# Kernel tuning notes

Hardware: AMD Instinct MI355X
Metric: run time of the kernel (lower is better)

The kernel has to match this reference:

```python
import jax, jax.numpy as jnp
import numpy as np

B, LX, LY, D = 8, 2048, 2048, 256

def setup_inputs() -> dict:
    key = jax.random.key(0)
    k1, k2, k3, k4 = jax.random.split(key, 4)
    x = jax.random.normal(k1, (B, LX, D), dtype=jnp.float32)
    y = jax.random.normal(k2, (B, LY, D), dtype=jnp.float32)
    y_mask = jax.random.randint(k3, (B, LY), 0, 2).astype(jnp.bool_)
    W = jax.random.normal(k4, (D, D), dtype=jnp.float32) * (1.0 / np.sqrt(D))
    b = jnp.zeros((D,), dtype=jnp.float32)
    return {"x": x, "y": y, "y_mask": y_mask, "W": W, "b": b}

def reference(x, y, y_mask, W, b):
    # shared linear + relu projection (torch Linear: x @ W.T + b)
    x_proj = jax.nn.relu(jnp.einsum('bld,ed->ble', x, W) + b)  # [B,LX,D]
    y_proj = jax.nn.relu(jnp.einsum('bld,ed->ble', y, W) + b)  # [B,LY,D]
    scores = jnp.einsum('bxd,byd->bxy', x_proj, y_proj)        # [B,LX,LY]
    scores = jnp.where(y_mask[:, None, :], -jnp.inf, scores)
    alpha = jax.nn.softmax(scores, axis=-1)                    # [B,LX,LY]
    return jnp.einsum('bxy,byd->bxd', alpha, y)                # [B,LX,D]
```

## Files before the change

### kernel.cpp

```cpp
#include <hip/hip_runtime.h>

typedef __attribute__((ext_vector_type(8))) short short8;
typedef _Float16 half8 __attribute__((ext_vector_type(8)));
typedef __attribute__((ext_vector_type(4))) float f32x4;
typedef __attribute__((ext_vector_type(4))) unsigned int uint4v;
typedef __attribute__((ext_vector_type(2))) unsigned int uint2v;

#define B_   8
#define LX_  2048
#define LY_  2048
#define D_   256
#define NROW (B_ * LX_)

__device__ __forceinline__ unsigned short f2bf(float f) {
  unsigned u = __builtin_bit_cast(unsigned, f);
  u += 0x7FFF + ((u >> 16) & 1);
  return (unsigned short)(u >> 16);
}
__device__ __forceinline__ float bf2f(unsigned short h) {
  unsigned u = ((unsigned)h) << 16;
  return __builtin_bit_cast(float, u);
}

__global__ __launch_bounds__(256) void prep_kernel(
    const float* __restrict__ W, unsigned short* __restrict__ Whi,
    unsigned short* __restrict__ Wlo,
    const int* __restrict__ MASK, int* __restrict__ CIDX, int* __restrict__ Lc) {
  int t = threadIdx.x;
  if (blockIdx.x >= 8) {
    int base = (blockIdx.x - 8) * 2048 + t * 8;
    f32x4 f0 = *(const f32x4*)(W + base);
    f32x4 f1 = *(const f32x4*)(W + base + 4);
    float v[8] = {f0[0], f0[1], f0[2], f0[3], f1[0], f1[1], f1[2], f1[3]};
    unsigned short h[8], l[8];
    for (int j = 0; j < 8; ++j) {
      h[j] = f2bf(v[j]);
      l[j] = f2bf(v[j] - bf2f(h[j]));
    }
    uint4v vh = {(unsigned)h[0] | ((unsigned)h[1] << 16), (unsigned)h[2] | ((unsigned)h[3] << 16),
                 (unsigned)h[4] | ((unsigned)h[5] << 16), (unsigned)h[6] | ((unsigned)h[7] << 16)};
    uint4v vl = {(unsigned)l[0] | ((unsigned)l[1] << 16), (unsigned)l[2] | ((unsigned)l[3] << 16),
                 (unsigned)l[4] | ((unsigned)l[5] << 16), (unsigned)l[6] | ((unsigned)l[7] << 16)};
    *(uint4v*)(Whi + base) = vh;
    *(uint4v*)(Wlo + base) = vl;
    return;
  }
  __shared__ int s[256];
  int b = blockIdx.x;
  int f[8];
  int cnt = 0;
  for (int k = 0; k < 8; ++k) {
    f[k] = (MASK[b * 2048 + t * 8 + k] == 0) ? 1 : 0;
    cnt += f[k];
  }
  s[t] = cnt;
  __syncthreads();
  for (int off = 1; off < 256; off <<= 1) {
    int v = (t >= off) ? s[t - off] : 0;
    __syncthreads();
    s[t] += v;
    __syncthreads();
  }
  if (t == 255) Lc[b] = s[255];
  int off = s[t] - cnt;
  for (int k = 0; k < 8; ++k) {
    int j = t * 8 + k;
    if (f[k]) CIDX[b * 2048 + (off++)] = j;
  }
}

__global__ __launch_bounds__(256, 2) void projgather_kernel(
    const float* __restrict__ X, const float* __restrict__ Y,
    const float* __restrict__ bias,
    const unsigned short* __restrict__ Whi, const unsigned short* __restrict__ Wlo,
    const int* __restrict__ CIDX, const int* __restrict__ Lc,
    _Float16* __restrict__ XP, _Float16* __restrict__ YPc,
    _Float16* __restrict__ YTc) {
  __shared__ __align__(16) unsigned char smem[51200];
  int t = threadIdx.x;

  if (blockIdx.x >= 512) {
    _Float16 (*tile)[72] = (_Float16(*)[72])smem;
    int id = blockIdx.x - 512;
    int db = id & 3, nb = (id >> 2) & 31, b = id >> 7;
    int lc = Lc[b];
    int end = (lc + 31) & ~31;
    if (nb * 64 >= end) return;
    int nl = t >> 2, ds = t & 3;
    int j = nb * 64 + nl;
    int idx = (j < lc) ? CIDX[b * 2048 + j] : 0;
    const float* src = Y + (size_t)(b * LY_ + idx) * D_ + db * 64 + ds * 16;
    for (int i = 0; i < 4; ++i) {
      f32x4 f = *(const f32x4*)(src + i * 4);
      for (int k = 0; k < 4; ++k) tile[ds * 16 + i * 4 + k][nl] = (_Float16)f[k];
    }
    __syncthreads();
    int dl = t >> 2, nsub = t & 3;
    uint4v v0 = *(const uint4v*)&tile[dl][nsub * 16];
    uint4v v1 = *(const uint4v*)&tile[dl][nsub * 16 + 8];
    _Float16* dst = YTc + (size_t)(b * D_ + db * 64 + dl) * LY_ + nb * 64 + nsub * 16;
    *(uint4v*)(dst) = v0;
    *(uint4v*)(dst + 8) = v1;
    return;
  }

  unsigned short (*Ah)[40] = (unsigned short(*)[40])(smem);
  unsigned short (*Al)[40] = (unsigned short(*)[40])(smem + 5120);
  unsigned short (*Bh)[40] = (unsigned short(*)[40])(smem + 10240);
  unsigned short (*Bl)[40] = (unsigned short(*)[40])(smem + 30720);

  int lane = t & 63, wave = t >> 6;
  int q = lane >> 4, n15 = lane & 15;
  int arow = t >> 2, aseg = t & 3;
  int erow = t >> 2, ec = t & 3;

  bool isX = blockIdx.x < 256;
  int m0 = 0, b = 0, slot0 = 0, lcb = 0;
  const float* arow_ptr;
  if (isX) {
    m0 = blockIdx.x * 64;
    arow_ptr = X + (size_t)(m0 + arow) * D_;
  } else {
    int id = blockIdx.x - 256;
    b = id >> 5;
    int rb = id & 31;
    lcb = Lc[b];
    slot0 = rb * 64;
    if (slot0 >= lcb) return;
    int sl = slot0 + arow;
    int grow = (sl < lcb) ? CIDX[b * 2048 + sl] : 0;
    arow_ptr = Y + (size_t)(b * 2048 + grow) * D_;
  }

  f32x4 acc[4][4];
  for (int mt = 0; mt < 4; ++mt)
    for (int nt = 0; nt < 4; ++nt) acc[mt][nt] = (f32x4){0.f, 0.f, 0.f, 0.f};

  f32x4 pa[2];
  uint4v pbh[4], pbl[4];
#define PROJ_PF(kc)                                                            \
  {                                                                            \
    for (int i = 0; i < 2; ++i)                                                \
      pa[i] = *(const f32x4*)(arow_ptr + (kc) * 32 + (aseg + i * 4) * 4);      \
    for (int p = 0; p < 4; ++p) {                                              \
      int e = p * 64 + erow;                                                   \
      pbh[p] = *(const uint4v*)(Whi + (size_t)e * D_ + (kc) * 32 + ec * 8);    \
      pbl[p] = *(const uint4v*)(Wlo + (size_t)e * D_ + (kc) * 32 + ec * 8);    \
    }                                                                          \
  }

  PROJ_PF(0);

  for (int kc = 0; kc < 8; ++kc) {
    __syncthreads();
    for (int i = 0; i < 2; ++i) {
      int seg = aseg + i * 4;
      f32x4 f = pa[i];
      unsigned short h[4], l[4];
      for (int j = 0; j < 4; ++j) {
        h[j] = f2bf(f[j]);
        l[j] = f2bf(f[j] - bf2f(h[j]));
      }
      uint2v vh = {(unsigned)h[0] | ((unsigned)h[1] << 16),
                   (unsigned)h[2] | ((unsigned)h[3] << 16)};
      uint2v vl = {(unsigned)l[0] | ((unsigned)l[1] << 16),
                   (unsigned)l[2] | ((unsigned)l[3] << 16)};
      *(uint2v*)&Ah[arow][seg * 4] = vh;
      *(uint2v*)&Al[arow][seg * 4] = vl;
    }
    for (int p = 0; p < 4; ++p) {
      int e = p * 64 + erow;
      *(uint4v*)&Bh[e][ec * 8] = pbh[p];
      *(uint4v*)&Bl[e][ec * 8] = pbl[p];
    }
    if (kc < 7) PROJ_PF(kc + 1);
    __syncthreads();

    short8 afh[4], afl[4], bfh[4], bfl[4];
    for (int mt = 0; mt < 4; ++mt) {
      afh[mt] = *(const short8*)&Ah[mt * 16 + n15][q * 8];
      afl[mt] = *(const short8*)&Al[mt * 16 + n15][q * 8];
    }
    for (int nt = 0; nt < 4; ++nt) {
      bfh[nt] = *(const short8*)&Bh[wave * 64 + nt * 16 + n15][q * 8];
      bfl[nt] = *(const short8*)&Bl[wave * 64 + nt * 16 + n15][q * 8];
    }
    for (int mt = 0; mt < 4; ++mt)
      for (int nt = 0; nt < 4; ++nt) {
        acc[mt][nt] = __builtin_amdgcn_mfma_f32_16x16x32_bf16(afh[mt], bfh[nt], acc[mt][nt], 0, 0, 0);
        acc[mt][nt] = __builtin_amdgcn_mfma_f32_16x16x32_bf16(afl[mt], bfh[nt], acc[mt][nt], 0, 0, 0);
        acc[mt][nt] = __builtin_amdgcn_mfma_f32_16x16x32_bf16(afh[mt], bfl[nt], acc[mt][nt], 0, 0, 0);
      }
  }
#undef PROJ_PF

  __syncthreads();
  _Float16 (*epi)[264] = (_Float16(*)[264])smem;
  for (int nt = 0; nt < 4; ++nt) {
    int e = wave * 64 + nt * 16 + n15;
    float bv = bias[e];
    for (int mt = 0; mt < 4; ++mt)
      for (int r = 0; r < 4; ++r) {
        float v = acc[mt][nt][r] + bv;
        v = v > 0.f ? v : 0.f;
        epi[mt * 16 + q * 4 + r][e] = (_Float16)v;
      }
  }
  __syncthreads();
  int row = t >> 2, seg = t & 3;
  bool valid = isX || (slot0 + row < lcb);
  if (valid) {
    _Float16* drp = isX ? (XP + (size_t)(m0 + row) * D_)
                        : (YPc + (size_t)(b * 2048 + slot0 + row) * D_);
    for (int k = 0; k < 8; ++k) {
      uint4v v = *(const uint4v*)&epi[row][seg * 64 + k * 8];
      *(uint4v*)(drp + seg * 64 + k * 8) = v;
    }
  }
}

__global__ __launch_bounds__(256, 3) void flash_kernel(
    const _Float16* __restrict__ XP, const _Float16* __restrict__ YPc,
    const _Float16* __restrict__ YTc, const int* __restrict__ Lc,
    _Float16* __restrict__ PO, float* __restrict__ Pm, float* __restrict__ Pl,
    int ns) {
  __shared__ __align__(16) _Float16 yp_t[32][264];
  __shared__ __align__(16) _Float16 yT_t[256][32];
  __shared__ __align__(16) _Float16 pbuf[4][16][40];

  int t = threadIdx.x;
  int lane = t & 63, wave = t >> 6;
  int q = lane >> 4, n15 = lane & 15;
  int p = blockIdx.x % ns;
  int rest = blockIdx.x / ns;
  int xb = rest & 31;
  int b = rest >> 5;
  int row0 = xb * 64 + wave * 16;

  int lc = Lc[b];
  int T  = (lc + 31) >> 5;
  int tstart = (T * p) / ns;
  int tend   = (T * (p + 1)) / ns;

  half8 a[8];
  const _Float16* xrow = XP + (size_t)(b * LX_ + row0 + n15) * D_ + q * 8;
  for (int kk = 0; kk < 8; ++kk) a[kk] = *(const half8*)(xrow + kk * 32);

  half8 lones;
  for (int j = 0; j < 8; ++j) lones[j] = (n15 == 0) ? (_Float16)1 : (_Float16)0;

  float m_r[4];
  for (int r = 0; r < 4; ++r) m_r[r] = -1e30f;
  f32x4 lacc = {0.f, 0.f, 0.f, 0.f};
  f32x4 oacc[16];
  for (int dt = 0; dt < 16; ++dt) oacc[dt] = (f32x4){0.f, 0.f, 0.f, 0.f};

  const _Float16* ypb = YPc + (size_t)b * LY_ * D_;
  const _Float16* yTb = YTc + (size_t)b * D_ * LY_;

  for (int tt = tstart; tt < tend; ++tt) {
    int y0 = tt * 32;
    uint4v ld[8];
    for (int i = 0; i < 4; ++i) {
      int c = t + i * 256;
      ld[i] = *(const uint4v*)(ypb + (size_t)(y0 + (c >> 5)) * D_ + (c & 31) * 8);
    }
    for (int i = 0; i < 4; ++i) {
      int c = t + i * 256;
      ld[4 + i] = *(const uint4v*)(yTb + (size_t)(c >> 2) * LY_ + y0 + (c & 3) * 8);
    }
    __syncthreads();
    for (int i = 0; i < 4; ++i) {
      int c = t + i * 256;
      *(uint4v*)&yp_t[c >> 5][(c & 31) * 8] = ld[i];
    }
    for (int i = 0; i < 4; ++i) {
      int c = t + i * 256;
      int rT = c >> 2, pc = (c & 3) ^ (rT & 3);
      *(uint4v*)&yT_t[rT][pc * 8] = ld[4 + i];
    }
    __syncthreads();

    f32x4 S0 = {0.f, 0.f, 0.f, 0.f}, S1 = {0.f, 0.f, 0.f, 0.f};
    for (int kk = 0; kk < 8; ++kk) {
      half8 b0 = *(const half8*)&yp_t[n15][kk * 32 + q * 8];
      S0 = __builtin_amdgcn_mfma_f32_16x16x32_f16(a[kk], b0, S0, 0, 0, 0);
    }
    for (int kk = 0; kk < 8; ++kk) {
      half8 b1 = *(const half8*)&yp_t[16 + n15][kk * 32 + q * 8];
      S1 = __builtin_amdgcn_mfma_f32_16x16x32_f16(a[kk], b1, S1, 0, 0, 0);
    }
    bool mk0 = (y0 + n15) >= lc;
    bool mk1 = (y0 + 16 + n15) >= lc;

    float al[4];
    _Float16 ph0[4], ph1[4];
    bool need = false;
    for (int r = 0; r < 4; ++r) {
      float s0 = mk0 ? -1e30f : S0[r];
      float s1 = mk1 ? -1e30f : S1[r];
      float tm = fmaxf(s0, s1);
      tm = fmaxf(tm, __shfl_xor(tm, 1));
      tm = fmaxf(tm, __shfl_xor(tm, 2));
      tm = fmaxf(tm, __shfl_xor(tm, 4));
      tm = fmaxf(tm, __shfl_xor(tm, 8));
      float mn = fmaxf(m_r[r], tm);
      al[r] = __expf(m_r[r] - mn);
      m_r[r] = mn;
      ph0[r] = (_Float16)__expf(s0 - mn);
      ph1[r] = (_Float16)__expf(s1 - mn);
      need = need || (al[r] != 1.0f);
    }
    if (__ballot(need)) {
      for (int dt = 0; dt < 16; ++dt)
        for (int r = 0; r < 4; ++r) oacc[dt][r] *= al[r];
      for (int r = 0; r < 4; ++r) lacc[r] *= al[r];
    }
    for (int r = 0; r < 4; ++r) {
      pbuf[wave][q * 4 + r][n15] = ph0[r];
      pbuf[wave][q * 4 + r][16 + n15] = ph1[r];
    }
    half8 pa = *(const half8*)&pbuf[wave][n15][q * 8];
    lacc = __builtin_amdgcn_mfma_f32_16x16x32_f16(pa, lones, lacc, 0, 0, 0);
    for (int dt = 0; dt < 16; ++dt) {
      int rT = dt * 16 + n15;
      half8 bb = *(const half8*)&yT_t[rT][(q ^ (rT & 3)) * 8];
      oacc[dt] = __builtin_amdgcn_mfma_f32_16x16x32_f16(pa, bb, oacc[dt], 0, 0, 0);
    }
  }

  size_t prow = (size_t)(p * B_ + b) * LX_ + row0;
  _Float16* po = PO + prow * D_;
  for (int dt = 0; dt < 16; ++dt)
    for (int r = 0; r < 4; ++r)
      po[(size_t)(q * 4 + r) * D_ + dt * 16 + n15] = (_Float16)oacc[dt][r];
  if (n15 == 0) {
    for (int r = 0; r < 4; ++r) {
      Pm[prow + q * 4 + r] = m_r[r];
      Pl[prow + q * 4 + r] = lacc[r];
    }
  }
}

__global__ __launch_bounds__(256) void merge_kernel(
    const _Float16* __restrict__ PO, const float* __restrict__ Pm,
    const float* __restrict__ Pl, float* __restrict__ OUT, int ns) {
  int c = blockIdx.x * 256 + threadIdx.x;
  int row = c >> 5, seg = c & 31;
  float m = Pm[row];
  for (int p = 1; p < ns; ++p) m = fmaxf(m, Pm[p * NROW + row]);
  float denom = 0.f;
  f32x4 o0 = {0.f, 0.f, 0.f, 0.f}, o1 = {0.f, 0.f, 0.f, 0.f};
  for (int p = 0; p < ns; ++p) {
    float w = __expf(Pm[p * NROW + row] - m);
    denom += Pl[p * NROW + row] * w;
    const _Float16* pp = PO + ((size_t)p * NROW + row) * D_ + seg * 8;
    half8 a = *(const half8*)pp;
    for (int j = 0; j < 4; ++j) o0[j] += (float)a[j] * w;
    for (int j = 0; j < 4; ++j) o1[j] += (float)a[4 + j] * w;
  }
  float inv = 1.0f / denom;
  for (int j = 0; j < 4; ++j) o0[j] *= inv;
  for (int j = 0; j < 4; ++j) o1[j] *= inv;
  float* o = OUT + (size_t)row * D_ + seg * 8;
  *(f32x4*)o = o0;
  *(f32x4*)(o + 4) = o1;
}

extern "C" void kernel_launch(void* const* d_in, const int* in_sizes, int n_in,
                              void* d_out, int out_size, void* d_ws, size_t ws_size,
                              hipStream_t stream) {
  const float* x     = (const float*)d_in[0];
  const float* y     = (const float*)d_in[1];
  const int*   ymask = (const int*)  d_in[2];
  const float* W     = (const float*)d_in[3];
  const float* bias  = (const float*)d_in[4];
  float* out = (float*)d_out;

  size_t need3 = 262144ull
               + 3ull * 8388608ull
               + 3ull * 8388608ull
               + 6ull * 65536ull
               + 65536ull + 4096ull;
  int ns = (ws_size >= need3) ? 3 : 2;

  char* ws = (char*)d_ws;
  size_t o = 0;
  unsigned short* Whi = (unsigned short*)(ws + o); o += 131072;
  unsigned short* Wlo = (unsigned short*)(ws + o); o += 131072;
  _Float16* XP  = (_Float16*)(ws + o); o += 8388608;
  _Float16* YPc = (_Float16*)(ws + o); o += 8388608;
  _Float16* YTc = (_Float16*)(ws + o); o += 8388608;
  _Float16* PO  = (_Float16*)(ws + o); o += (size_t)ns * 8388608;
  float* Pm   = (float*)(ws + o); o += (size_t)ns * 65536;
  float* Pl   = (float*)(ws + o); o += (size_t)ns * 65536;
  int*   CIDX = (int*)  (ws + o); o += 65536;
  int*   Lc   = (int*)  (ws + o);

  prep_kernel<<<40, 256, 0, stream>>>(W, Whi, Wlo, ymask, CIDX, Lc);
  projgather_kernel<<<1536, 256, 0, stream>>>(x, y, bias, Whi, Wlo, CIDX, Lc,
                                              XP, YPc, YTc);
  flash_kernel<<<256 * ns, 256, 0, stream>>>(XP, YPc, YTc, Lc, PO, Pm, Pl, ns);
  merge_kernel<<<2048, 256, 0, stream>>>(PO, Pm, Pl, out, ns);
}
```

Measured before the change: 160.7 us.

## Prefetch next Y tile into registers and compute row sums with scalar adds

Global loads for the next 32-row Y tile are issued into registers right after the current tile is written to shared memory, so their latency overlaps the score, softmax and PV MFMAs. The row-sum denominator is now kept per lane in fp32 as a running sum of the unrounded exponentials, replacing the MFMA against a ones vector, and is reduced with shuffles once at the end. This keeps eight more vector registers live across the loop, which may reduce occupancy. It also adds per-iteration scalar FMAs that run on every tile, not only when the ballot says a rescale is needed.

```diff
diff --git a/kernel.cpp b/kernel.cpp
--- a/kernel.cpp
+++ b/kernel.cpp
@@ -246,9 +246,6 @@
   const _Float16* xrow = XP + (size_t)(b * LX_ + row0 + n15) * D_ + q * 8;
   for (int kk = 0; kk < 8; ++kk) a[kk] = *(const half8*)(xrow + kk * 32);
 
-  half8 lones;
-  for (int j = 0; j < 8; ++j) lones[j] = (n15 == 0) ? (_Float16)1 : (_Float16)0;
-
   float m_r[4];
   for (int r = 0; r < 4; ++r) m_r[r] = -1e30f;
   f32x4 lacc = {0.f, 0.f, 0.f, 0.f};
@@ -258,27 +255,35 @@
   const _Float16* ypb = YPc + (size_t)b * LY_ * D_;
   const _Float16* yTb = YTc + (size_t)b * D_ * LY_;
 
+  uint4v pr[8];
+#define PREFETCH(tt)                                                          \
+  {                                                                           \
+    int y0p = (tt) * 32;                                                      \
+    for (int i = 0; i < 4; ++i) {                                             \
+      int c = t + i * 256;                                                    \
+      pr[i] = *(const uint4v*)(ypb + (size_t)(y0p + (c >> 5)) * D_ + (c & 31) * 8); \
+    }                                                                         \
+    for (int i = 0; i < 4; ++i) {                                             \
+      int c = t + i * 256;                                                    \
+      pr[4 + i] = *(const uint4v*)(yTb + (size_t)(c >> 2) * LY_ + y0p + (c & 3) * 8); \
+    }                                                                         \
+  }
+
+  if (tstart < tend) PREFETCH(tstart);
+
   for (int tt = tstart; tt < tend; ++tt) {
     int y0 = tt * 32;
-    uint4v ld[8];
+    __syncthreads();
     for (int i = 0; i < 4; ++i) {
       int c = t + i * 256;
-      ld[i] = *(const uint4v*)(ypb + (size_t)(y0 + (c >> 5)) * D_ + (c & 31) * 8);
-    }
-    for (int i = 0; i < 4; ++i) {
-      int c = t + i * 256;
-      ld[4 + i] = *(const uint4v*)(yTb + (size_t)(c >> 2) * LY_ + y0 + (c & 3) * 8);
-    }
-    __syncthreads();
-    for (int i = 0; i < 4; ++i) {
-      int c = t + i * 256;
-      *(uint4v*)&yp_t[c >> 5][(c & 31) * 8] = ld[i];
+      *(uint4v*)&yp_t[c >> 5][(c & 31) * 8] = pr[i];
     }
     for (int i = 0; i < 4; ++i) {
       int c = t + i * 256;
       int rT = c >> 2, pc = (c & 3) ^ (rT & 3);
-      *(uint4v*)&yT_t[rT][pc * 8] = ld[4 + i];
-    }
+      *(uint4v*)&yT_t[rT][pc * 8] = pr[4 + i];
+    }
+    if (tt + 1 < tend) PREFETCH(tt + 1);
     __syncthreads();
 
     f32x4 S0 = {0.f, 0.f, 0.f, 0.f}, S1 = {0.f, 0.f, 0.f, 0.f};
@@ -307,33 +312,43 @@
       float mn = fmaxf(m_r[r], tm);
       al[r] = __expf(m_r[r] - mn);
       m_r[r] = mn;
-      ph0[r] = (_Float16)__expf(s0 - mn);
-      ph1[r] = (_Float16)__expf(s1 - mn);
+      float p0f = __expf(s0 - mn);
+      float p1f = __expf(s1 - mn);
+      ph0[r] = (_Float16)p0f;
+      ph1[r] = (_Float16)p1f;
+      lacc[r] = lacc[r] * al[r] + p0f + p1f;
       need = need || (al[r] != 1.0f);
     }
     if (__ballot(need)) {
       for (int dt = 0; dt < 16; ++dt)
         for (int r = 0; r < 4; ++r) oacc[dt][r] *= al[r];
-      for (int r = 0; r < 4; ++r) lacc[r] *= al[r];
     }
     for (int r = 0; r < 4; ++r) {
       pbuf[wave][q * 4 + r][n15] = ph0[r];
       pbuf[wave][q * 4 + r][16 + n15] = ph1[r];
     }
     half8 pa = *(const half8*)&pbuf[wave][n15][q * 8];
-    lacc = __builtin_amdgcn_mfma_f32_16x16x32_f16(pa, lones, lacc, 0, 0, 0);
     for (int dt = 0; dt < 16; ++dt) {
       int rT = dt * 16 + n15;
       half8 bb = *(const half8*)&yT_t[rT][(q ^ (rT & 3)) * 8];
       oacc[dt] = __builtin_amdgcn_mfma_f32_16x16x32_f16(pa, bb, oacc[dt], 0, 0, 0);
     }
   }
+#undef PREFETCH
 
   size_t prow = (size_t)(p * B_ + b) * LX_ + row0;
   _Float16* po = PO + prow * D_;
   for (int dt = 0; dt < 16; ++dt)
     for (int r = 0; r < 4; ++r)
       po[(size_t)(q * 4 + r) * D_ + dt * 16 + n15] = (_Float16)oacc[dt][r];
+  for (int r = 0; r < 4; ++r) {
+    float v = lacc[r];
+    v += __shfl_xor(v, 1);
+    v += __shfl_xor(v, 2);
+    v += __shfl_xor(v, 4);
+    v += __shfl_xor(v, 8);
+    lacc[r] = v;
+  }
   if (n15 == 0) {
     for (int r = 0; r < 4; ++r) {
       Pm[prow + q * 4 + r] = m_r[r];
```

New measurement: 192.7 us. 19.9% more time.
